# Performance work log

Hardware: AMD Instinct MI355X
Metric: run time of the kernel (lower is better)

## Reference

```python
import jax, jax.numpy as jnp
import numpy as np

TAU = 0.5
LOGIT_TAU = float(np.log(TAU / (1.0 - TAU)))  # = 0.0 for tau=0.5
N_STEPS = 128           # torch samples randint(128,129) -> always 128
N_SECANT = 8
D_MIN, D_MAX = 0.0, 2.4
B, N, HID, CDIM = 4, 8192, 64, 128


def decoder(p, c, W1, Wc, b1, W2, b2):
    """Occupancy-logit MLP. p: (B, ..., 3), c: (B, CDIM) -> (B, ...)."""
    cc = c @ Wc  # (B, HID)
    cc = cc.reshape(cc.shape[:1] + (1,) * (p.ndim - 2) + cc.shape[1:])
    h = jax.nn.relu(jnp.einsum('...d,dh->...h', p, W1) + cc + b1)
    return (h @ W2 + b2)[..., 0]


def setup_inputs() -> dict:
    key = jax.random.key(0)
    ks = jax.random.split(key, 8)
    return {
        'ray0': jax.random.normal(ks[0], (B, N, 3), jnp.float32) * 0.5,
        'ray_direction': jax.random.normal(ks[1], (B, N, 3), jnp.float32),
        'c': jax.random.normal(ks[2], (B, CDIM), jnp.float32),
        'W1': jax.random.normal(ks[3], (3, HID), jnp.float32) * 0.5,
        'Wc': jax.random.normal(ks[4], (CDIM, HID), jnp.float32) * 0.1,
        'b1': jax.random.normal(ks[5], (HID,), jnp.float32) * 0.1,
        'W2': jax.random.normal(ks[6], (HID, 1), jnp.float32) * 0.5,
        'b2': jax.random.normal(ks[7], (1,), jnp.float32) * 0.1,
    }


def reference(ray0, ray_direction, c, W1, Wc, b1, W2, b2):
    S = N_STEPS
    bsz, npts, _ = ray0.shape
    dec = lambda p: decoder(p, c, W1, Wc, b1, W2, b2)

    # --- coarse ray marching ---
    d_prop = jnp.linspace(D_MIN, D_MAX, S).astype(ray0.dtype)        # (S,)
    p_prop = ray0[:, :, None, :] + ray_direction[:, :, None, :] * d_prop[None, None, :, None]
    val = dec(p_prop) - LOGIT_TAU                                    # (B, N, S)

    mask_0_not_occupied = val[:, :, 0] < 0
    sign_matrix = jnp.concatenate(
        [jnp.sign(val[:, :, :-1] * val[:, :, 1:]),
         jnp.ones((bsz, npts, 1), val.dtype)], axis=-1)
    cost_matrix = sign_matrix * jnp.arange(S, 0, -1, dtype=val.dtype)
    indices = jnp.argmin(cost_matrix, axis=-1)                       # (B, N)
    values = jnp.min(cost_matrix, axis=-1)
    mask_sign_change = values < 0
    f_low = jnp.take_along_axis(val, indices[..., None], axis=2)[..., 0]
    mask_neg_to_pos = f_low < 0
    mask = mask_sign_change & mask_neg_to_pos & mask_0_not_occupied

    d_prop_full = jnp.broadcast_to(d_prop, (bsz, npts, S))
    d_low = jnp.take_along_axis(d_prop_full, indices[..., None], axis=2)[..., 0]
    idx_hi = jnp.minimum(indices + 1, S - 1)
    d_high = jnp.take_along_axis(d_prop_full, idx_hi[..., None], axis=2)[..., 0]
    f_high = jnp.take_along_axis(val, idx_hi[..., None], axis=2)[..., 0]

    # safe placeholders for non-surface rays (results discarded by mask)
    d_low = jnp.where(mask, d_low, 0.0)
    d_high = jnp.where(mask, d_high, 1.0)
    f_low = jnp.where(mask, f_low, -1.0)
    f_high = jnp.where(mask, f_high, 1.0)

    # --- secant refinement (vectorized over all rays) ---
    d_pred = -f_low * (d_high - d_low) / (f_high - f_low) + d_low
    for _ in range(N_SECANT):
        p_mid = ray0 + d_pred[..., None] * ray_direction
        f_mid = dec(p_mid) - LOGIT_TAU
        ind_low = f_mid < 0
        d_low = jnp.where(ind_low, d_pred, d_low)
        f_low = jnp.where(ind_low, f_mid, f_low)
        d_high = jnp.where(ind_low, d_high, d_pred)
        f_high = jnp.where(ind_low, f_high, f_mid)
        d_pred = -f_low * (d_high - d_low) / (f_high - f_low) + d_low

    d_out = jnp.where(mask, d_pred, jnp.inf)
    d_out = jnp.where(mask_0_not_occupied, d_out, 0.0)
    return d_out
```

## Files before the change

### kernel.cpp

```cpp
#include <hip/hip_runtime.h>
#include <hip/hip_bf16.h>

#define HID   64
#define CDIM  128
#define NSTEP 128
#define NRAYS 32768

typedef const __hip_bfloat16* __restrict__ bf16p;

#define WS_CCB  0
#define WS_WX   256
#define WS_WY   320
#define WS_WZ   384
#define WS_W2   448
#define WS_CNT  512
#define QID     1024
#define QDL     (QID + 32768)
#define QDH     (QDL + 32768)
#define QFL     (QDH + 32768)
#define QFH     (QFL + 32768)

__device__ __forceinline__ float bf2f(__hip_bfloat16 x) { return __bfloat162float(x); }

__global__ void precompute_cc(bf16p c, bf16p Wc, bf16p b1, bf16p W1, bf16p W2,
                              float* __restrict__ ws) {
    __shared__ float part[4][HID];
    int b = blockIdx.x;
    int h = threadIdx.x & 63;
    int q = threadIdx.x >> 6;
    float acc = 0.0f;
    const __hip_bfloat16* crow = c + b * CDIM;
#pragma unroll
    for (int k = q * 32; k < q * 32 + 32; ++k)
        acc = fmaf(bf2f(crow[k]), bf2f(Wc[k * HID + h]), acc);
    part[q][h] = acc;
    if (b == 0) {
        if (q == 1) {
            ws[WS_WX + h] = bf2f(W1[h]);
            ws[WS_WY + h] = bf2f(W1[HID + h]);
        } else if (q == 2) {
            ws[WS_WZ + h] = bf2f(W1[2 * HID + h]);
            ws[WS_W2 + h] = bf2f(W2[h]);
        } else if (q == 3 && h < 4) {
            ((int*)ws)[WS_CNT + h] = 0;
        }
    }
    __syncthreads();
    if (q == 0)
        ws[WS_CCB + b * HID + h] =
            bf2f(b1[h]) + ((part[0][h] + part[1][h]) + (part[2][h] + part[3][h]));
}

__global__ __launch_bounds__(256) void raymarch(
    bf16p ray0, bf16p rdir, bf16p b2,
    float* __restrict__ ws, __hip_bfloat16* __restrict__ out) {
    __shared__ float2 sAB[4][HID];

    const int tid  = threadIdx.x;
    const int wave = tid >> 6;
    const int lane = tid & 63;
    const int r    = blockIdx.x * 4 + wave;
    const int batch = blockIdx.x >> 11;

    const float ox = bf2f(ray0[r * 3 + 0]), oy = bf2f(ray0[r * 3 + 1]), oz = bf2f(ray0[r * 3 + 2]);
    const float dx = bf2f(rdir[r * 3 + 0]), dy = bf2f(rdir[r * 3 + 1]), dz = bf2f(rdir[r * 3 + 2]);
    const float b2v = bf2f(b2[0]);

    {
        const float wx = ws[WS_WX + lane];
        const float wy = ws[WS_WY + lane];
        const float wz = ws[WS_WZ + lane];
        const float cb = ws[WS_CCB + batch * HID + lane];
        float alpha = fmaf(ox, wx, fmaf(oy, wy, fmaf(oz, wz, cb)));
        float beta  = fmaf(dx, wx, fmaf(dy, wy, dz * wz));
        sAB[wave][lane] = make_float2(alpha, beta);
    }

    const float STEPF = 2.4f / 127.0f;
    const float d0 = bf2f(__float2bfloat16(lane * STEPF));
    const float d1 = bf2f(__float2bfloat16((lane + 64) * STEPF));

    const float* __restrict__ W2F = ws + WS_W2;
    float a0 = b2v, a1 = b2v;
#pragma unroll 8
    for (int j = 0; j < HID; ++j) {
        const float2 ab = sAB[wave][j];
        const float  w2 = W2F[j];
        float h0 = fmaf(d0, ab.y, ab.x);
        float h1 = fmaf(d1, ab.y, ab.x);
        a0 = fmaf(fmaxf(h0, 0.0f), w2, a0);
        a1 = fmaf(fmaxf(h1, 0.0f), w2, a1);
    }
    float val0 = a0, val1 = a1;

    float v1l0  = __shfl(val1, 0);
    float valn0 = __shfl_down(val0, 1);
    valn0 = (lane == 63) ? v1l0 : valn0;
    float valn1 = __shfl_down(val1, 1);

    float prod0 = val0 * valn0;
    float sgn0  = (prod0 < 0.0f) ? -1.0f : ((prod0 > 0.0f) ? 1.0f : 0.0f);
    float cost0 = sgn0 * (float)(128 - lane);
    float prod1 = val1 * valn1;
    float sgn1  = (prod1 < 0.0f) ? -1.0f : ((prod1 > 0.0f) ? 1.0f : 0.0f);
    float cost1 = (lane == 63) ? 1.0f : sgn1 * (float)(64 - lane);

    float key0 = fmaf(cost0, 256.0f, (float)lane);
    float key1 = fmaf(cost1, 256.0f, (float)(lane + 64));
    float k = fminf(key0, key1);
#pragma unroll
    for (int off = 32; off > 0; off >>= 1)
        k = fminf(k, __shfl_xor(k, off));
    const float cf = floorf(k * 0.00390625f);
    const int   mi = (int)(k - cf * 256.0f);

    const int idx  = mi;
    const int idxh = (idx + 1 < NSTEP) ? idx + 1 : NSTEP - 1;

    float va  = __shfl(val0, idx  & 63);
    float vb  = __shfl(val1, idx  & 63);
    float f_low  = (idx  < 64) ? va  : vb;
    float vah = __shfl(val0, idxh & 63);
    float vbh = __shfl(val1, idxh & 63);
    float f_high = (idxh < 64) ? vah : vbh;

    float v00 = __shfl(val0, 0);
    bool  m0   = v00 < 0.0f;
    bool  mask = (cf < 0.0f) && (f_low < 0.0f) && m0;

    if (lane == 0) {
        if (mask) {
            int pos = atomicAdd((int*)ws + WS_CNT + batch, 1);
            int qo  = batch * 8192 + pos;
            ((int*)ws)[QID + qo] = r;
            ws[QDL + qo] = bf2f(__float2bfloat16(idx  * STEPF));
            ws[QDH + qo] = bf2f(__float2bfloat16(idxh * STEPF));
            ws[QFL + qo] = f_low;
            ws[QFH + qo] = f_high;
        } else {
            out[r] = __float2bfloat16(m0 ? 0x1.FEp127f : 0.0f);
        }
    }
}

__global__ __launch_bounds__(256) void secant(
    bf16p ray0, bf16p rdir, bf16p b2,
    const float* __restrict__ ws, __hip_bfloat16* __restrict__ out) {
    const int gtid  = blockIdx.x * 256 + threadIdx.x;
    const int batch = gtid >> 13;
    const int i     = gtid & 8191;
    const int cnt   = ((const int*)ws)[WS_CNT + batch];
    if (i >= cnt) return;

    const int qo  = batch * 8192 + i;
    const int rid = ((const int*)ws)[QID + qo];
    float dl = ws[QDL + qo], dh = ws[QDH + qo];
    float fl = ws[QFL + qo], fh = ws[QFH + qo];

    const float ox = bf2f(ray0[rid * 3 + 0]), oy = bf2f(ray0[rid * 3 + 1]), oz = bf2f(ray0[rid * 3 + 2]);
    const float dx = bf2f(rdir[rid * 3 + 0]), dy = bf2f(rdir[rid * 3 + 1]), dz = bf2f(rdir[rid * 3 + 2]);
    const float b2v = bf2f(b2[0]);

    const float* __restrict__ WXF = ws + WS_WX;
    const float* __restrict__ WYF = ws + WS_WY;
    const float* __restrict__ WZF = ws + WS_WZ;
    const float* __restrict__ W2F = ws + WS_W2;
    const float* __restrict__ CBF = ws + WS_CCB + batch * HID;

    float dp = -fl * (dh - dl) / (fh - fl) + dl;
#pragma unroll
    for (int it = 0; it < 8; ++it) {
        float px = fmaf(dp, dx, ox), py = fmaf(dp, dy, oy), pz = fmaf(dp, dz, oz);
        float acc = b2v;
#pragma unroll 8
        for (int j = 0; j < HID; ++j) {
            float h = fmaf(px, WXF[j], fmaf(py, WYF[j], fmaf(pz, WZF[j], CBF[j])));
            acc = fmaf(fmaxf(h, 0.0f), W2F[j], acc);
        }
        bool lowside = acc < 0.0f;
        dl = lowside ? dp : dl;
        fl = lowside ? acc : fl;
        dh = lowside ? dh : dp;
        fh = lowside ? fh : acc;
        dp = -fl * (dh - dl) / (fh - fl) + dl;
    }
    out[rid] = __float2bfloat16(dp);
}

extern "C" void kernel_launch(void* const* d_in, const int* in_sizes, int n_in,
                              void* d_out, int out_size, void* d_ws, size_t ws_size,
                              hipStream_t stream) {
    bf16p ray0 = (bf16p)d_in[0];
    bf16p rdir = (bf16p)d_in[1];
    bf16p c    = (bf16p)d_in[2];
    bf16p W1   = (bf16p)d_in[3];
    bf16p Wc   = (bf16p)d_in[4];
    bf16p b1   = (bf16p)d_in[5];
    bf16p W2   = (bf16p)d_in[6];
    bf16p b2   = (bf16p)d_in[7];
    __hip_bfloat16* out = (__hip_bfloat16*)d_out;
    float* ws = (float*)d_ws;

    hipLaunchKernelGGL(precompute_cc, dim3(4), dim3(256), 0, stream, c, Wc, b1, W1, W2, ws);
    hipLaunchKernelGGL(raymarch, dim3(NRAYS / 4), dim3(256), 0, stream,
                       ray0, rdir, b2, ws, out);
    hipLaunchKernelGGL(secant, dim3(128), dim3(256), 0, stream,
                       ray0, rdir, b2, ws, out);
}
```

Measured before the change: 90.84 us.

## Process four rays per wave with eight march steps per lane in registers

Each wave now handles four rays instead of one: 16 lanes per ray, each lane computing eight consecutive march samples in registers. A single LDS load of the per-ray alpha/beta pair and the W2 weight is reused across eight samples, cutting LDS and weight-load traffic per FMA. The argmin reduction shrinks to a 16-lane shuffle tree, and f_low/f_high are found with an in-register select plus one shuffle. Register pressure rises and the grid is four times smaller, which may reduce occupancy.

```diff
diff --git a/kernel.cpp b/kernel.cpp
--- a/kernel.cpp
+++ b/kernel.cpp
@@ -54,81 +54,98 @@
 __global__ __launch_bounds__(256) void raymarch(
     bf16p ray0, bf16p rdir, bf16p b2,
     float* __restrict__ ws, __hip_bfloat16* __restrict__ out) {
-    __shared__ float2 sAB[4][HID];
+    __shared__ float2 sAB[4][HID][4];
 
     const int tid  = threadIdx.x;
     const int wave = tid >> 6;
     const int lane = tid & 63;
-    const int r    = blockIdx.x * 4 + wave;
-    const int batch = blockIdx.x >> 11;
-
-    const float ox = bf2f(ray0[r * 3 + 0]), oy = bf2f(ray0[r * 3 + 1]), oz = bf2f(ray0[r * 3 + 2]);
-    const float dx = bf2f(rdir[r * 3 + 0]), dy = bf2f(rdir[r * 3 + 1]), dz = bf2f(rdir[r * 3 + 2]);
+    const int rbase = blockIdx.x * 16 + wave * 4;
+    const int batch = blockIdx.x >> 9;
+
     const float b2v = bf2f(b2[0]);
+    const float STEPF = 2.4f / 127.0f;
 
     {
         const float wx = ws[WS_WX + lane];
         const float wy = ws[WS_WY + lane];
         const float wz = ws[WS_WZ + lane];
         const float cb = ws[WS_CCB + batch * HID + lane];
-        float alpha = fmaf(ox, wx, fmaf(oy, wy, fmaf(oz, wz, cb)));
-        float beta  = fmaf(dx, wx, fmaf(dy, wy, dz * wz));
-        sAB[wave][lane] = make_float2(alpha, beta);
-    }
-
-    const float STEPF = 2.4f / 127.0f;
-    const float d0 = bf2f(__float2bfloat16(lane * STEPF));
-    const float d1 = bf2f(__float2bfloat16((lane + 64) * STEPF));
-
-    const float* __restrict__ W2F = ws + WS_W2;
-    float a0 = b2v, a1 = b2v;
-#pragma unroll 8
+        float a[4], bb[4];
+#pragma unroll
+        for (int t = 0; t < 4; ++t) {
+            const int r = rbase + t;
+            const float ox = bf2f(ray0[r * 3 + 0]), oy = bf2f(ray0[r * 3 + 1]), oz = bf2f(ray0[r * 3 + 2]);
+            const float dx = bf2f(rdir[r * 3 + 0]), dy = bf2f(rdir[r * 3 + 1]), dz = bf2f(rdir[r * 3 + 2]);
+            a[t]  = fmaf(ox, wx, fmaf(oy, wy, fmaf(oz, wz, cb)));
+            bb[t] = fmaf(dx, wx, fmaf(dy, wy, dz * wz));
+        }
+        float4* dst = (float4*)&sAB[wave][lane][0];
+        dst[0] = make_float4(a[0], bb[0], a[1], bb[1]);
+        dst[1] = make_float4(a[2], bb[2], a[3], bb[3]);
+    }
+
+    const int t = lane >> 4;
+    const int g = lane & 15;
+
+    float d[8], v[8];
+#pragma unroll
+    for (int k = 0; k < 8; ++k) {
+        d[k] = bf2f(__float2bfloat16((float)(8 * g + k) * STEPF));
+        v[k] = b2v;
+    }
+
+    const float* __restrict__ W2R = ws + WS_W2;
+    const float2* __restrict__ abp = &sAB[wave][0][t];
+#pragma unroll
     for (int j = 0; j < HID; ++j) {
-        const float2 ab = sAB[wave][j];
-        const float  w2 = W2F[j];
-        float h0 = fmaf(d0, ab.y, ab.x);
-        float h1 = fmaf(d1, ab.y, ab.x);
-        a0 = fmaf(fmaxf(h0, 0.0f), w2, a0);
-        a1 = fmaf(fmaxf(h1, 0.0f), w2, a1);
-    }
-    float val0 = a0, val1 = a1;
-
-    float v1l0  = __shfl(val1, 0);
-    float valn0 = __shfl_down(val0, 1);
-    valn0 = (lane == 63) ? v1l0 : valn0;
-    float valn1 = __shfl_down(val1, 1);
-
-    float prod0 = val0 * valn0;
-    float sgn0  = (prod0 < 0.0f) ? -1.0f : ((prod0 > 0.0f) ? 1.0f : 0.0f);
-    float cost0 = sgn0 * (float)(128 - lane);
-    float prod1 = val1 * valn1;
-    float sgn1  = (prod1 < 0.0f) ? -1.0f : ((prod1 > 0.0f) ? 1.0f : 0.0f);
-    float cost1 = (lane == 63) ? 1.0f : sgn1 * (float)(64 - lane);
-
-    float key0 = fmaf(cost0, 256.0f, (float)lane);
-    float key1 = fmaf(cost1, 256.0f, (float)(lane + 64));
-    float k = fminf(key0, key1);
-#pragma unroll
-    for (int off = 32; off > 0; off >>= 1)
-        k = fminf(k, __shfl_xor(k, off));
-    const float cf = floorf(k * 0.00390625f);
-    const int   mi = (int)(k - cf * 256.0f);
+        const float2 ab = abp[j * 4];
+        const float  w2 = W2R[j];
+#pragma unroll
+        for (int k = 0; k < 8; ++k) {
+            float h = fmaf(d[k], ab.y, ab.x);
+            v[k] = fmaf(fmaxf(h, 0.0f), w2, v[k]);
+        }
+    }
+
+    float nv = __shfl_down(v[0], 1);
+    float key;
+#pragma unroll
+    for (int k = 0; k < 8; ++k) {
+        const int s = 8 * g + k;
+        float vn = (k < 7) ? v[k + 1] : nv;
+        float prod = v[k] * vn;
+        float sgn = (prod < 0.0f) ? -1.0f : ((prod > 0.0f) ? 1.0f : 0.0f);
+        float kk = (s == NSTEP - 1) ? (256.0f + 127.0f)
+                                    : fmaf(sgn * (float)(NSTEP - s), 256.0f, (float)s);
+        key = (k == 0) ? kk : fminf(key, kk);
+    }
+#pragma unroll
+    for (int off = 1; off < 16; off <<= 1)
+        key = fminf(key, __shfl_xor(key, off));
+    const float cf = floorf(key * 0.00390625f);
+    const int   mi = (int)(key - cf * 256.0f);
 
     const int idx  = mi;
     const int idxh = (idx + 1 < NSTEP) ? idx + 1 : NSTEP - 1;
-
-    float va  = __shfl(val0, idx  & 63);
-    float vb  = __shfl(val1, idx  & 63);
-    float f_low  = (idx  < 64) ? va  : vb;
-    float vah = __shfl(val0, idxh & 63);
-    float vbh = __shfl(val1, idxh & 63);
-    float f_high = (idxh < 64) ? vah : vbh;
-
-    float v00 = __shfl(val0, 0);
-    bool  m0   = v00 < 0.0f;
-    bool  mask = (cf < 0.0f) && (f_low < 0.0f) && m0;
-
-    if (lane == 0) {
+    const int q  = idx  & 7, qh = idxh & 7;
+
+    float cand = v[0], candh = v[0];
+#pragma unroll
+    for (int k = 1; k < 8; ++k) {
+        cand  = (q  == k) ? v[k] : cand;
+        candh = (qh == k) ? v[k] : candh;
+    }
+    const int lane_lo = (lane & 48) | (idx  >> 3);
+    const int lane_hi = (lane & 48) | (idxh >> 3);
+    float f_low  = __shfl(cand,  lane_lo);
+    float f_high = __shfl(candh, lane_hi);
+    float v00    = __shfl(v[0], lane & 48);
+
+    bool m0   = v00 < 0.0f;
+    bool mask = (key < 0.0f) && (f_low < 0.0f) && m0;
+
+    if (g == 0) {
+        const int r = rbase + t;
         if (mask) {
             int pos = atomicAdd((int*)ws + WS_CNT + batch, 1);
             int qo  = batch * 8192 + pos;
@@ -202,7 +219,7 @@
     float* ws = (float*)d_ws;
 
     hipLaunchKernelGGL(precompute_cc, dim3(4), dim3(256), 0, stream, c, Wc, b1, W1, W2, ws);
-    hipLaunchKernelGGL(raymarch, dim3(NRAYS / 4), dim3(256), 0, stream,
+    hipLaunchKernelGGL(raymarch, dim3(NRAYS / 16), dim3(256), 0, stream,
                        ray0, rdir, b2, ws, out);
     hipLaunchKernelGGL(secant, dim3(128), dim3(256), 0, stream,
                        ray0, rdir, b2, ws, out);
```

New measurement: 89.76 us. About the same (-1.2%).
